# Kernel optimization log

Measured on AMD Instinct MI355X. Metric: run time of the kernel, lower is better.

The kernel has to match this reference:

```python
import jax, jax.numpy as jnp
import numpy as np
import math

B, T, C, H = 16384, 64, 48, 48


def setup_inputs() -> dict:
    key = jax.random.key(0)
    kx, kq, kk, kv = jax.random.split(key, 4)
    return {
        "x": jax.random.normal(kx, (B, T, C), dtype=jnp.float32),
        "Wq": jax.random.normal(kq, (C, H), dtype=jnp.float32) * 0.02,
        "Wk": jax.random.normal(kk, (C, H), dtype=jnp.float32) * 0.02,
        "Wv": jax.random.normal(kv, (C, H), dtype=jnp.float32) * 0.02,
    }


def reference(x, Wq, Wk, Wv):
    # x: [B, T, C]; projections (Linear with bias=False): [B, T, H]
    q = x @ Wq
    k = x @ Wk
    v = x @ Wv
    scale = 1.0 / math.sqrt(H)
    # scores: [B, T, T]
    wei = jnp.einsum("bth,bsh->bts", q, k) * scale
    causal = jnp.tril(jnp.ones((T, T), dtype=bool))  # tril mask, T==BLOCK_SIZE
    wei = jnp.where(causal, wei, -jnp.inf)
    wei = jax.nn.softmax(wei, axis=-1)
    # dropout is identity in eval mode
    return jnp.einsum("bts,bsh->bth", wei, v)
```

## Files before the change

kernel.cpp:

```cpp
#include <hip/hip_runtime.h>
#include <math.h>

typedef __bf16 bf16x8 __attribute__((ext_vector_type(8)));
typedef float f32x4 __attribute__((ext_vector_type(4)));
typedef unsigned short u16;

#define LD 72

__device__ __forceinline__ u16 f2b(float f) {
  unsigned u = __builtin_bit_cast(unsigned, f);
  u = (u + 0x7fffu + ((u >> 16) & 1u)) >> 16;
  return (u16)u;
}

__device__ __forceinline__ f32x4 mfma16(bf16x8 a, bf16x8 b, f32x4 c) {
  return __builtin_amdgcn_mfma_f32_16x16x32_bf16(a, b, c, 0, 0, 0);
}

__global__ __launch_bounds__(256) void head_prep(const float* __restrict__ Wq,
                                                 const float* __restrict__ Wk,
                                                 const float* __restrict__ Wv,
                                                 u16* __restrict__ ws) {
  const float scale = 0.14433756729740643f;
  for (int idx = threadIdx.x; idx < 48 * LD; idx += 256) {
    int r = idx / LD;
    int c = idx % LD;
    float mv = 0.f, wv = 0.f;
    if (c < 48) {
      float acc = 0.f;
      for (int h = 0; h < 48; ++h) acc += Wq[c * 48 + h] * Wk[r * 48 + h];
      mv = acc * scale;
      wv = Wv[c * 48 + r];
    }
    ws[idx] = f2b(mv);
    ws[48 * LD + idx] = f2b(wv);
  }
}

__global__ __launch_bounds__(256, 4) void head_main(const float* __restrict__ x,
                                                    const u16* __restrict__ wimg,
                                                    float* __restrict__ out) {
  __shared__ u16 lds[272 * LD];
  u16* const W_M = lds;
  u16* const W_V = lds + 48 * LD;
  u16* const X   = lds + 96 * LD;
  u16* const QM  = lds + 160 * LD;
  u16* const VT  = lds + 224 * LD;

  const int tid  = threadIdx.x;
  const int lane = tid & 63;
  const int w    = tid >> 6;
  const int qd   = lane >> 4;
  const int col  = lane & 15;
  const long b   = blockIdx.x;

  {
    const uint4* src = (const uint4*)wimg;
    uint4* dst = (uint4*)lds;
    #pragma unroll
    for (int i = 0; i < 4; ++i) {
      int idx = tid + i * 256;
      if (idx < (96 * LD * 2) / 16) dst[idx] = src[idx];
    }
  }
  {
    const float* xb = x + b * 3072;
    #pragma unroll
    for (int it = 0; it < 3; ++it) {
      int flat = tid * 4 + it * 1024;
      float4 v = *(const float4*)(xb + flat);
      int row = flat / 48;
      int c0  = flat % 48;
      ushort4 pk;
      pk.x = f2b(v.x); pk.y = f2b(v.y); pk.z = f2b(v.z); pk.w = f2b(v.w);
      *(ushort4*)(X + row * LD + c0) = pk;
    }
    int zr = tid >> 2;
    int zc = 48 + (tid & 3) * 6;
    #pragma unroll
    for (int j = 0; j < 6; ++j) {
      X[zr * LD + zc + j] = 0;
      QM[zr * LD + zc + j] = 0;
    }
  }
  __syncthreads();

  {
    const int arow = (16 * w + col) * LD + qd * 8;
    bf16x8 xa0 = *(const bf16x8*)(X + arow);
    bf16x8 xa1 = *(const bf16x8*)(X + arow + 32);
    #pragma unroll
    for (int n = 0; n < 3; ++n) {
      const int brow = (16 * n + col) * LD + qd * 8;
      f32x4 av = {0.f, 0.f, 0.f, 0.f};
      f32x4 aq = {0.f, 0.f, 0.f, 0.f};
      av = mfma16(xa0, *(const bf16x8*)(W_V + brow), av);
      av = mfma16(xa1, *(const bf16x8*)(W_V + brow + 32), av);
      aq = mfma16(xa0, *(const bf16x8*)(W_M + brow), aq);
      aq = mfma16(xa1, *(const bf16x8*)(W_M + brow + 32), aq);
      ushort4 pv;
      pv.x = f2b(av[0]); pv.y = f2b(av[1]); pv.z = f2b(av[2]); pv.w = f2b(av[3]);
      *(ushort4*)(VT + (16 * n + col) * LD + 16 * w + qd * 4) = pv;
      #pragma unroll
      for (int i = 0; i < 4; ++i)
        QM[(16 * w + qd * 4 + i) * LD + 16 * n + col] = f2b(aq[i]);
    }
  }
  __syncthreads();

  float sv[4][4];
  {
    const int arow = (16 * w + col) * LD + qd * 8;
    bf16x8 qa0 = *(const bf16x8*)(QM + arow);
    bf16x8 qa1 = *(const bf16x8*)(QM + arow + 32);
    #pragma unroll
    for (int st = 0; st < 4; ++st) {
      const int brow = (16 * st + col) * LD + qd * 8;
      f32x4 a = {0.f, 0.f, 0.f, 0.f};
      a = mfma16(qa0, *(const bf16x8*)(X + brow), a);
      a = mfma16(qa1, *(const bf16x8*)(X + brow + 32), a);
      #pragma unroll
      for (int i = 0; i < 4; ++i) sv[st][i] = a[i];
    }
  }

  float m4[4] = {-INFINITY, -INFINITY, -INFINITY, -INFINITY};
  #pragma unroll
  for (int st = 0; st < 4; ++st) {
    #pragma unroll
    for (int i = 0; i < 4; ++i) {
      int tg = 16 * w + qd * 4 + i;
      int sg = 16 * st + col;
      float v = (sg <= tg) ? sv[st][i] : -INFINITY;
      sv[st][i] = v;
      m4[i] = fmaxf(m4[i], v);
    }
  }
  #pragma unroll
  for (int d = 1; d < 16; d <<= 1) {
    #pragma unroll
    for (int i = 0; i < 4; ++i) m4[i] = fmaxf(m4[i], __shfl_xor(m4[i], d, 64));
  }
  float l4[4] = {0.f, 0.f, 0.f, 0.f};
  #pragma unroll
  for (int st = 0; st < 4; ++st) {
    #pragma unroll
    for (int i = 0; i < 4; ++i) {
      float p = __expf(sv[st][i] - m4[i]);
      sv[st][i] = p;
      l4[i] += p;
    }
  }
  #pragma unroll
  for (int d = 1; d < 16; d <<= 1) {
    #pragma unroll
    for (int i = 0; i < 4; ++i) l4[i] += __shfl_xor(l4[i], d, 64);
  }

  __syncthreads();

  u16* const Pw = X + w * 16 * LD;
  #pragma unroll
  for (int st = 0; st < 4; ++st) {
    #pragma unroll
    for (int i = 0; i < 4; ++i)
      Pw[(qd * 4 + i) * LD + 16 * st + col] = f2b(sv[st][i]);
  }

  f32x4 o0 = {0.f, 0.f, 0.f, 0.f}, o1 = o0, o2 = o0;
  #pragma unroll
  for (int kt = 0; kt < 2; ++kt) {
    bf16x8 pa = *(const bf16x8*)(Pw + col * LD + qd * 8 + 32 * kt);
    o0 = mfma16(pa, *(const bf16x8*)(VT + (0  + col) * LD + qd * 8 + 32 * kt), o0);
    o1 = mfma16(pa, *(const bf16x8*)(VT + (16 + col) * LD + qd * 8 + 32 * kt), o1);
    o2 = mfma16(pa, *(const bf16x8*)(VT + (32 + col) * LD + qd * 8 + 32 * kt), o2);
  }
  float rl[4];
  #pragma unroll
  for (int i = 0; i < 4; ++i) rl[i] = __builtin_amdgcn_rcpf(l4[i]);

  float* ob = out + b * 3072 + (16 * w + qd * 4) * 48 + col;
  #pragma unroll
  for (int i = 0; i < 4; ++i) {
    ob[i * 48 +  0] = o0[i] * rl[i];
    ob[i * 48 + 16] = o1[i] * rl[i];
    ob[i * 48 + 32] = o2[i] * rl[i];
  }
}

extern "C" void kernel_launch(void* const* d_in, const int* in_sizes, int n_in,
                              void* d_out, int out_size, void* d_ws, size_t ws_size,
                              hipStream_t stream) {
  const float* x  = (const float*)d_in[0];
  const float* Wq = (const float*)d_in[1];
  const float* Wk = (const float*)d_in[2];
  const float* Wv = (const float*)d_in[3];
  u16* wimg = (u16*)d_ws;
  head_prep<<<1, 256, 0, stream>>>(Wq, Wk, Wv, wimg);
  head_main<<<16384, 256, 0, stream>>>(x, wimg, (float*)d_out);
}
```

Baseline: 370.4 us.

## Swizzle LDS layout, alias Q into weight region, shrink LDS for occupancy

Replaces the padded LD=72 shared-memory rows with 64-wide rows using an XOR swizzle on 8-element chunks, so MFMA operand loads avoid bank conflicts without padding. Q·M is kept in registers and written over the weight region after a barrier, which removes the separate QM buffer and cuts LDS from 272 to 208 rows. This lets launch bounds rise to 6 blocks per CU. The prep kernel also stages the weights in shared memory and writes the pre-swizzled image. The cost is extra index arithmetic, plus reliance on __threadfence_block instead of barriers for wave-private regions.

```diff
diff --git a/kernel.cpp b/kernel.cpp
--- a/kernel.cpp
+++ b/kernel.cpp
@@ -4,8 +4,6 @@
 typedef __bf16 bf16x8 __attribute__((ext_vector_type(8)));
 typedef float f32x4 __attribute__((ext_vector_type(4)));
 typedef unsigned short u16;
-
-#define LD 72
 
 __device__ __forceinline__ u16 f2b(float f) {
   unsigned u = __builtin_bit_cast(unsigned, f);
@@ -17,35 +15,48 @@
   return __builtin_amdgcn_mfma_f32_16x16x32_bf16(a, b, c, 0, 0, 0);
 }
 
+__device__ __forceinline__ int sw(int r, int c) {
+  return (r << 6) + ((((c >> 3) ^ r) & 7) << 3) + (c & 7);
+}
+__device__ __forceinline__ int swc(int r, int ch) {
+  return (r << 6) + (((ch ^ r) & 7) << 3);
+}
+
 __global__ __launch_bounds__(256) void head_prep(const float* __restrict__ Wq,
                                                  const float* __restrict__ Wk,
                                                  const float* __restrict__ Wv,
                                                  u16* __restrict__ ws) {
+  __shared__ float wq[2304], wk[2304], wv[2304];
   const float scale = 0.14433756729740643f;
-  for (int idx = threadIdx.x; idx < 48 * LD; idx += 256) {
-    int r = idx / LD;
-    int c = idx % LD;
-    float mv = 0.f, wv = 0.f;
+  for (int i = threadIdx.x; i < 2304; i += 256) {
+    wq[i] = Wq[i];
+    wk[i] = Wk[i];
+    wv[i] = Wv[i];
+  }
+  __syncthreads();
+  for (int idx = threadIdx.x; idx < 96 * 64; idx += 256) {
+    int r = idx >> 6, c = idx & 63;
+    float v = 0.f;
     if (c < 48) {
-      float acc = 0.f;
-      for (int h = 0; h < 48; ++h) acc += Wq[c * 48 + h] * Wk[r * 48 + h];
-      mv = acc * scale;
-      wv = Wv[c * 48 + r];
-    }
-    ws[idx] = f2b(mv);
-    ws[48 * LD + idx] = f2b(wv);
-  }
-}
-
-__global__ __launch_bounds__(256, 4) void head_main(const float* __restrict__ x,
+      if (r < 48) {
+        float a = 0.f;
+        for (int h = 0; h < 48; ++h) a += wq[c * 48 + h] * wk[r * 48 + h];
+        v = a * scale;
+      } else {
+        v = wv[c * 48 + (r - 48)];
+      }
+    }
+    ws[sw(r, c)] = f2b(v);
+  }
+}
+
+__global__ __launch_bounds__(256, 6) void head_main(const float* __restrict__ x,
                                                     const u16* __restrict__ wimg,
                                                     float* __restrict__ out) {
-  __shared__ u16 lds[272 * LD];
-  u16* const W_M = lds;
-  u16* const W_V = lds + 48 * LD;
-  u16* const X   = lds + 96 * LD;
-  u16* const QM  = lds + 160 * LD;
-  u16* const VT  = lds + 224 * LD;
+  __shared__ u16 lds[208 * 64];
+  u16* const R0 = lds;
+  u16* const X  = lds + 96 * 64;
+  u16* const VT = lds + 160 * 64;
 
   const int tid  = threadIdx.x;
   const int lane = tid & 63;
@@ -57,15 +68,13 @@
   {
     const uint4* src = (const uint4*)wimg;
     uint4* dst = (uint4*)lds;
-    #pragma unroll
-    for (int i = 0; i < 4; ++i) {
-      int idx = tid + i * 256;
-      if (idx < (96 * LD * 2) / 16) dst[idx] = src[idx];
-    }
+    dst[tid]       = src[tid];
+    dst[tid + 256] = src[tid + 256];
+    dst[tid + 512] = src[tid + 512];
   }
   {
     const float* xb = x + b * 3072;
-    #pragma unroll
+#pragma unroll
     for (int it = 0; it < 3; ++it) {
       int flat = tid * 4 + it * 1024;
       float4 v = *(const float4*)(xb + flat);
@@ -73,61 +82,68 @@
       int c0  = flat % 48;
       ushort4 pk;
       pk.x = f2b(v.x); pk.y = f2b(v.y); pk.z = f2b(v.z); pk.w = f2b(v.w);
-      *(ushort4*)(X + row * LD + c0) = pk;
+      *(ushort4*)(X + sw(row, c0)) = pk;
     }
     int zr = tid >> 2;
-    int zc = 48 + (tid & 3) * 6;
-    #pragma unroll
-    for (int j = 0; j < 6; ++j) {
-      X[zr * LD + zc + j] = 0;
-      QM[zr * LD + zc + j] = 0;
-    }
-  }
-  __syncthreads();
-
-  {
-    const int arow = (16 * w + col) * LD + qd * 8;
-    bf16x8 xa0 = *(const bf16x8*)(X + arow);
-    bf16x8 xa1 = *(const bf16x8*)(X + arow + 32);
-    #pragma unroll
+    int zq = tid & 3;
+    ushort4 z = {0, 0, 0, 0};
+    *(ushort4*)(X + swc(zr, 6 + (zq >> 1)) + (zq & 1) * 4) = z;
+  }
+  __syncthreads();
+
+  f32x4 aq[3];
+  {
+    const int ar = 16 * w + col;
+    const bf16x8 xa0 = *(const bf16x8*)(X + swc(ar, qd));
+    const bf16x8 xa1 = *(const bf16x8*)(X + swc(ar, qd + 4));
+    const u16* WM = R0;
+    const u16* WV = R0 + 48 * 64;
+#pragma unroll
     for (int n = 0; n < 3; ++n) {
-      const int brow = (16 * n + col) * LD + qd * 8;
+      const int br = 16 * n + col;
+      const int b0 = swc(br, qd);
+      const int b1 = swc(br, qd + 4);
       f32x4 av = {0.f, 0.f, 0.f, 0.f};
-      f32x4 aq = {0.f, 0.f, 0.f, 0.f};
-      av = mfma16(xa0, *(const bf16x8*)(W_V + brow), av);
-      av = mfma16(xa1, *(const bf16x8*)(W_V + brow + 32), av);
-      aq = mfma16(xa0, *(const bf16x8*)(W_M + brow), aq);
-      aq = mfma16(xa1, *(const bf16x8*)(W_M + brow + 32), aq);
+      av = mfma16(xa0, *(const bf16x8*)(WV + b0), av);
+      av = mfma16(xa1, *(const bf16x8*)(WV + b1), av);
+      f32x4 a = {0.f, 0.f, 0.f, 0.f};
+      a = mfma16(xa0, *(const bf16x8*)(WM + b0), a);
+      a = mfma16(xa1, *(const bf16x8*)(WM + b1), a);
+      aq[n] = a;
       ushort4 pv;
       pv.x = f2b(av[0]); pv.y = f2b(av[1]); pv.z = f2b(av[2]); pv.w = f2b(av[3]);
-      *(ushort4*)(VT + (16 * n + col) * LD + 16 * w + qd * 4) = pv;
-      #pragma unroll
-      for (int i = 0; i < 4; ++i)
-        QM[(16 * w + qd * 4 + i) * LD + 16 * n + col] = f2b(aq[i]);
-    }
-  }
-  __syncthreads();
+      *(ushort4*)(VT + sw(16 * n + col, 16 * w + qd * 4)) = pv;
+    }
+  }
+  __syncthreads();
+
+#pragma unroll
+  for (int n = 0; n < 3; ++n)
+#pragma unroll
+    for (int i = 0; i < 4; ++i)
+      R0[sw(16 * w + qd * 4 + i, 16 * n + col)] = f2b(aq[n][i]);
+  __threadfence_block();
 
   float sv[4][4];
   {
-    const int arow = (16 * w + col) * LD + qd * 8;
-    bf16x8 qa0 = *(const bf16x8*)(QM + arow);
-    bf16x8 qa1 = *(const bf16x8*)(QM + arow + 32);
-    #pragma unroll
+    const int ar = 16 * w + col;
+    const bf16x8 qa0 = *(const bf16x8*)(R0 + swc(ar, qd));
+    const bf16x8 qa1 = *(const bf16x8*)(R0 + swc(ar, qd + 4));
+#pragma unroll
     for (int st = 0; st < 4; ++st) {
-      const int brow = (16 * st + col) * LD + qd * 8;
+      const int br = 16 * st + col;
       f32x4 a = {0.f, 0.f, 0.f, 0.f};
-      a = mfma16(qa0, *(const bf16x8*)(X + brow), a);
-      a = mfma16(qa1, *(const bf16x8*)(X + brow + 32), a);
-      #pragma unroll
+      a = mfma16(qa0, *(const bf16x8*)(X + swc(br, qd)), a);
+      a = mfma16(qa1, *(const bf16x8*)(X + swc(br, qd + 4)), a);
+#pragma unroll
       for (int i = 0; i < 4; ++i) sv[st][i] = a[i];
     }
   }
 
   float m4[4] = {-INFINITY, -INFINITY, -INFINITY, -INFINITY};
-  #pragma unroll
-  for (int st = 0; st < 4; ++st) {
-    #pragma unroll
+#pragma unroll
+  for (int st = 0; st < 4; ++st)
+#pragma unroll
     for (int i = 0; i < 4; ++i) {
       int tg = 16 * w + qd * 4 + i;
       int sg = 16 * st + col;
@@ -135,52 +151,51 @@
       sv[st][i] = v;
       m4[i] = fmaxf(m4[i], v);
     }
-  }
-  #pragma unroll
-  for (int d = 1; d < 16; d <<= 1) {
-    #pragma unroll
+#pragma unroll
+  for (int d = 1; d < 16; d <<= 1)
+#pragma unroll
     for (int i = 0; i < 4; ++i) m4[i] = fmaxf(m4[i], __shfl_xor(m4[i], d, 64));
-  }
   float l4[4] = {0.f, 0.f, 0.f, 0.f};
-  #pragma unroll
-  for (int st = 0; st < 4; ++st) {
-    #pragma unroll
+#pragma unroll
+  for (int st = 0; st < 4; ++st)
+#pragma unroll
     for (int i = 0; i < 4; ++i) {
       float p = __expf(sv[st][i] - m4[i]);
       sv[st][i] = p;
       l4[i] += p;
     }
-  }
-  #pragma unroll
-  for (int d = 1; d < 16; d <<= 1) {
-    #pragma unroll
+#pragma unroll
+  for (int d = 1; d < 16; d <<= 1)
+#pragma unroll
     for (int i = 0; i < 4; ++i) l4[i] += __shfl_xor(l4[i], d, 64);
-  }
-
-  __syncthreads();
-
-  u16* const Pw = X + w * 16 * LD;
-  #pragma unroll
-  for (int st = 0; st < 4; ++st) {
-    #pragma unroll
+
+  __syncthreads();
+
+#pragma unroll
+  for (int st = 0; st < 4; ++st)
+#pragma unroll
     for (int i = 0; i < 4; ++i)
-      Pw[(qd * 4 + i) * LD + 16 * st + col] = f2b(sv[st][i]);
-  }
+      X[sw(16 * w + qd * 4 + i, 16 * st + col)] = f2b(sv[st][i]);
+  __threadfence_block();
 
   f32x4 o0 = {0.f, 0.f, 0.f, 0.f}, o1 = o0, o2 = o0;
-  #pragma unroll
-  for (int kt = 0; kt < 2; ++kt) {
-    bf16x8 pa = *(const bf16x8*)(Pw + col * LD + qd * 8 + 32 * kt);
-    o0 = mfma16(pa, *(const bf16x8*)(VT + (0  + col) * LD + qd * 8 + 32 * kt), o0);
-    o1 = mfma16(pa, *(const bf16x8*)(VT + (16 + col) * LD + qd * 8 + 32 * kt), o1);
-    o2 = mfma16(pa, *(const bf16x8*)(VT + (32 + col) * LD + qd * 8 + 32 * kt), o2);
+  {
+    const int pr = 16 * w + col;
+#pragma unroll
+    for (int kt = 0; kt < 2; ++kt) {
+      const int ch = qd + 4 * kt;
+      bf16x8 pa = *(const bf16x8*)(X + swc(pr, ch));
+      o0 = mfma16(pa, *(const bf16x8*)(VT + swc(0  + col, ch)), o0);
+      o1 = mfma16(pa, *(const bf16x8*)(VT + swc(16 + col, ch)), o1);
+      o2 = mfma16(pa, *(const bf16x8*)(VT + swc(32 + col, ch)), o2);
+    }
   }
   float rl[4];
-  #pragma unroll
+#pragma unroll
   for (int i = 0; i < 4; ++i) rl[i] = __builtin_amdgcn_rcpf(l4[i]);
 
   float* ob = out + b * 3072 + (16 * w + qd * 4) * 48 + col;
-  #pragma unroll
+#pragma unroll
   for (int i = 0; i < 4; ++i) {
     ob[i * 48 +  0] = o0[i] * rl[i];
     ob[i * 48 + 16] = o1[i] * rl[i];
```

New measurement: 340.6 us. 1.09x faster.
